# Kernel tuning notes

Measured on AMD Instinct MI355X. Metric: run time of the kernel, lower is better.

Reference implementation:

```python
import jax, jax.numpy as jnp
import numpy as np

D_STATE = 4
DT_RANK = 4  # ceil(64/16)
D_INNER = 64


def conv1d(x, w, b, pad):
    # x: [B,C,L], w: [O,I,K]
    y = jax.lax.conv_general_dilated(x, w, (1,), [(pad, pad)],
                                     dimension_numbers=('NCH', 'OIH', 'NCH'))
    return y + b[None, :, None]


def maxpool2(x):
    B, C, L = x.shape
    return x.reshape(B, C, L // 2, 2).max(-1)


def layernorm(x, g, b):
    m = x.mean(-1, keepdims=True)
    v = ((x - m) ** 2).mean(-1, keepdims=True)
    return (x - m) / jnp.sqrt(v + 1e-5) * g + b


def mamba_block(x, in_w, cv_w, cv_b, xp_w, dt_w, dt_b, A_log, Dp, out_w):
    # x: [B,L,d_model]; d_inner == d_model (expand=1)
    B, L, _ = x.shape
    xz = jnp.einsum('bld,ed->ble', x, in_w)          # [B,L,2*d_inner]
    xi, z = jnp.split(xz, 2, axis=-1)
    # causal depthwise conv, kernel size 2
    xc = jax.lax.conv_general_dilated(xi.transpose(0, 2, 1), cv_w, (1,), [(1, 0)],
                                      feature_group_count=D_INNER,
                                      dimension_numbers=('NCH', 'OIH', 'NCH'))
    u = jax.nn.silu(xc + cv_b[None, :, None]).transpose(0, 2, 1)  # [B,L,d_inner]
    x_dbl = jnp.einsum('bld,ed->ble', u, xp_w)        # [B,L,dt_rank+2*d_state]
    dt, Bm, Cm = jnp.split(x_dbl, [DT_RANK, DT_RANK + D_STATE], axis=-1)
    dt = jax.nn.softplus(jnp.einsum('blr,dr->bld', dt, dt_w) + dt_b)  # [B,L,d_inner]
    A = -jnp.exp(A_log)                               # [d_inner, d_state]
    dA = jnp.exp(dt[..., None] * A)                   # [B,L,d_inner,d_state]
    dBu = dt[..., None] * Bm[:, :, None, :] * u[..., None]

    def step(h, inp):
        dA_t, dBu_t, C_t = inp
        h = dA_t * h + dBu_t                          # [B,d_inner,d_state]
        y = jnp.einsum('bdn,bn->bd', h, C_t)
        return h, y

    h0 = jnp.zeros((B, D_INNER, D_STATE), x.dtype)
    _, ys = jax.lax.scan(step, h0, (dA.transpose(1, 0, 2, 3),
                                    dBu.transpose(1, 0, 2, 3),
                                    Cm.transpose(1, 0, 2)))
    y = ys.transpose(1, 0, 2) + Dp * u                # skip connection D*u
    y = y * jax.nn.silu(z)
    return jnp.einsum('bld,ed->ble', y, out_w)


def setup_inputs() -> dict:
    key = jax.random.key(0)
    ks = jax.random.split(key, 32)
    n = lambda k, s, sc=0.05: (jax.random.normal(k, s, jnp.float32) * sc)
    inp = {
        'x': jax.random.normal(ks[0], (512, 1, 4096), jnp.float32),
        'c1w': n(ks[1], (16, 1, 5), 0.3), 'c1b': n(ks[2], (16,)),
        'c2w': n(ks[3], (32, 16, 5), 0.1), 'c2b': n(ks[4], (32,)),
        'c3w': n(ks[5], (64, 32, 5), 0.08), 'c3b': n(ks[6], (64,)),
        'lw': n(ks[7], (4096, 2048), 0.02), 'lb': n(ks[8], (4096,)),
    }
    A_init = jnp.log(jnp.tile(jnp.arange(1, D_STATE + 1, dtype=jnp.float32), (D_INNER, 1)))
    for i, base in ((1, 9), (2, 20)):
        inp[f'ln{i}g'] = jnp.ones((64,), jnp.float32)
        inp[f'ln{i}b'] = jnp.zeros((64,), jnp.float32)
        inp[f'in{i}w'] = n(ks[base + 0], (2 * D_INNER, 64), 0.08)
        inp[f'cv{i}w'] = n(ks[base + 1], (D_INNER, 1, 2), 0.3)
        inp[f'cv{i}b'] = n(ks[base + 2], (D_INNER,))
        inp[f'xp{i}w'] = n(ks[base + 3], (DT_RANK + 2 * D_STATE, D_INNER), 0.08)
        inp[f'dt{i}w'] = n(ks[base + 4], (D_INNER, DT_RANK), 0.3)
        inp[f'dt{i}b'] = n(ks[base + 5], (D_INNER,), 0.5)
        inp[f'al{i}'] = A_init
        inp[f'dp{i}'] = jnp.ones((D_INNER,), jnp.float32)
        inp[f'ow{i}'] = n(ks[base + 6], (64, D_INNER), 0.08)
    return inp


def reference(x, c1w, c1b, c2w, c2b, c3w, c3b, lw, lb,
              ln1g, ln1b, in1w, cv1w, cv1b, xp1w, dt1w, dt1b, al1, dp1, ow1,
              ln2g, ln2b, in2w, cv2w, cv2b, xp2w, dt2w, dt2b, al2, dp2, ow2):
    B = x.shape[0]
    h = maxpool2(jax.nn.relu(conv1d(x, c1w, c1b, 2)))       # [B,16,L/2]
    h = maxpool2(jax.nn.relu(conv1d(h, c2w, c2b, 2)))       # [B,32,L/4]
    h = jax.nn.relu(conv1d(h, c3w, c3b, 2))                 # [B,64,L/4]
    # AdaptiveAvgPool1d(32): L/4 divisible by 32 -> exact window means
    L4 = h.shape[-1]
    h = h.reshape(B, 64, 32, L4 // 32).mean(-1)             # [B,64,32]
    h = h.reshape(B, -1)                                    # [B,2048]
    h = (h @ lw.T + lb).reshape(B, 64, 64)                  # [B,64,64]
    h = mamba_block(layernorm(h, ln1g, ln1b), in1w, cv1w, cv1b, xp1w, dt1w, dt1b, al1, dp1, ow1)
    h = mamba_block(layernorm(h, ln2g, ln2b), in2w, cv2w, cv2b, xp2w, dt2w, dt2b, al2, dp2, ow2)
    return h
```

## Files before the change

### kernel.cpp

```cpp
#include <hip/hip_runtime.h>
#include <hip/hip_bf16.h>
#include <math.h>

#define NB 512

typedef __attribute__((ext_vector_type(8))) short short8;
typedef __attribute__((ext_vector_type(4))) float f32x4;
union U4 { uint4 u; short8 s8; };
union BF { __hip_bfloat16 h; ushort us; };

__device__ __forceinline__ int swz(int u) { return u ^ ((u >> 3) & 7); }
__device__ __forceinline__ int idx8(int l, int u) { return l * 8 + (u ^ (l & 7)); }

__global__ __launch_bounds__(256) void prep_w(const float* __restrict__ w2,
                                              __hip_bfloat16* __restrict__ w2b,
                                              const float* __restrict__ w3,
                                              __hip_bfloat16* __restrict__ w3b,
                                              const float* __restrict__ in1w,
                                              const float* __restrict__ in2w,
                                              __hip_bfloat16* __restrict__ winb,
                                              const float* __restrict__ ow1,
                                              const float* __restrict__ ow2,
                                              __hip_bfloat16* __restrict__ owb) {
    int i = blockIdx.x * 256 + threadIdx.x;
    if (i < 3072) {
        int c2 = i / 96, rest = i - c2 * 96;
        int tp = rest >> 5, r2 = rest & 31;
        int tl = r2 >> 4, c1 = r2 & 15;
        int tap = tp * 2 + tl;
        float v = (tap < 5) ? w2[c2 * 80 + c1 * 5 + tap] : 0.f;
        w2b[i] = __float2bfloat16(v);
    } else if (i < 13312) {
        int j = i - 3072;
        int c3 = j / 160, rest = j - c3 * 160;
        int kk = rest >> 5, c1 = rest & 31;
        w3b[j] = __float2bfloat16(w3[c3 * 160 + c1 * 5 + kk]);
    } else if (i < 29696) {
        int j = i - 13312;
        winb[j] = __float2bfloat16((j < 8192 ? in1w : in2w)[j & 8191]);
    } else {
        int j = i - 29696;
        owb[j] = __float2bfloat16((j < 4096 ? ow1 : ow2)[j & 4095]);
    }
}

__global__ __launch_bounds__(256) void conv_trunk(const float* __restrict__ x,
                                                  const float* __restrict__ c1w,
                                                  const float* __restrict__ c1b,
                                                  const __hip_bfloat16* __restrict__ w2b,
                                                  const float* __restrict__ c2b,
                                                  const __hip_bfloat16* __restrict__ w3b,
                                                  const float* __restrict__ c3b,
                                                  __hip_bfloat16* __restrict__ h3b) {
    __shared__ uint4 H1u[1088];
    __shared__ uint4 H2u[1088];
    float* xs = (float*)H2u;
    int t = threadIdx.x, h = blockIdx.x, b = blockIdx.y;
    int lane = t & 63, w = t >> 6, m = lane & 15, quad = lane >> 4;
    int p0 = h * 512 - 6;
    int gbase = h * 1024 - 14;

    const float* xb = x + b * 4096;
    for (int i = t; i < 1080; i += 256) {
        int gx = gbase + i;
        xs[i] = (gx >= 0 && gx < 4096) ? xb[gx] : 0.f;
    }
    U4 Bf2[3][2];
    {
        const uint4* wsrc = (const uint4*)w2b;
#pragma unroll
        for (int ct = 0; ct < 2; ++ct)
#pragma unroll
            for (int tp = 0; tp < 3; ++tp)
                Bf2[tp][ct].u = wsrc[(ct * 16 + m) * 12 + tp * 4 + quad];
    }
    float bv2[2];
#pragma unroll
    for (int ct = 0; ct < 2; ++ct) bv2[ct] = c2b[ct * 16 + m];
    float wv[80], bv1[16];
#pragma unroll
    for (int i = 0; i < 80; ++i) wv[i] = c1w[i];
#pragma unroll
    for (int i = 0; i < 16; ++i) bv1[i] = c1b[i];
    __syncthreads();

    for (int r = t; r < 536; r += 256) {
        int p = p0 + r;
        union { uint4 q[2]; __hip_bfloat16 hh[16]; } o;
        if (p >= 0 && p < 2048) {
            const float* s = xs + 2 * r;
            float s0 = s[0], s1 = s[1], s2 = s[2], s3 = s[3], s4 = s[4], s5 = s[5];
#pragma unroll
            for (int c = 0; c < 16; ++c) {
                const float* wr = wv + c * 5;
                float v0 = fmaf(wr[0], s0, fmaf(wr[1], s1, fmaf(wr[2], s2, fmaf(wr[3], s3, fmaf(wr[4], s4, bv1[c])))));
                float v1 = fmaf(wr[0], s1, fmaf(wr[1], s2, fmaf(wr[2], s3, fmaf(wr[3], s4, fmaf(wr[4], s5, bv1[c])))));
                o.hh[c] = __float2bfloat16(fmaxf(fmaxf(v0, v1), 0.f));
            }
        } else {
            o.q[0] = (uint4){0, 0, 0, 0};
            o.q[1] = (uint4){0, 0, 0, 0};
        }
        H1u[swz(2 * r)] = o.q[0];
        H1u[swz(2 * r + 1)] = o.q[1];
    }
    __syncthreads();

    __hip_bfloat16* H2h = (__hip_bfloat16*)H2u;
    for (int g = w; g < 33; g += 4) {
        f32x4 acc[2];
#pragma unroll
        for (int ct = 0; ct < 2; ++ct) acc[ct] = (f32x4){bv2[ct], bv2[ct], bv2[ct], bv2[ct]};
#pragma unroll
        for (int tp = 0; tp < 3; ++tp) {
            int u = 2 * (g * 16 + m + 2 * tp) + quad;
            U4 av; av.u = H1u[swz(u)];
            acc[0] = __builtin_amdgcn_mfma_f32_16x16x32_bf16(av.s8, Bf2[tp][0].s8, acc[0], 0, 0, 0);
            acc[1] = __builtin_amdgcn_mfma_f32_16x16x32_bf16(av.s8, Bf2[tp][1].s8, acc[1], 0, 0, 0);
        }
        int pp = g * 8 + quad * 2;
#pragma unroll
        for (int ct = 0; ct < 2; ++ct) {
            float o0 = fmaxf(fmaxf(acc[ct][0], acc[ct][1]), 0.f);
            float o1 = fmaxf(fmaxf(acc[ct][2], acc[ct][3]), 0.f);
            int ch = ct * 16 + m;
            int u0 = pp * 4 + (ch >> 3);
            H2h[swz(u0) * 8 + (ch & 7)] = __float2bfloat16(o0);
            H2h[swz(u0 + 4) * 8 + (ch & 7)] = __float2bfloat16(o1);
        }
    }
    __syncthreads();
    if (h == 0 && t < 8) H2u[swz((t >> 2) * 4 + (t & 3))] = (uint4){0, 0, 0, 0};
    if (h == 3 && t < 8) H2u[swz((258 + (t >> 2)) * 4 + (t & 3))] = (uint4){0, 0, 0, 0};
    __syncthreads();

    U4 Bf3[5][4];
    {
        const uint4* wsrc = (const uint4*)w3b;
#pragma unroll
        for (int ct = 0; ct < 4; ++ct)
#pragma unroll
            for (int kk = 0; kk < 5; ++kk)
                Bf3[kk][ct].u = wsrc[(ct * 16 + m) * 20 + kk * 4 + quad];
    }
    float bv3[4];
#pragma unroll
    for (int ct = 0; ct < 4; ++ct) bv3[ct] = c3b[ct * 16 + m];

#pragma unroll
    for (int ww = 0; ww < 2; ++ww) {
        int wl = w * 2 + ww;
        float sum[4] = {0.f, 0.f, 0.f, 0.f};
#pragma unroll
        for (int half = 0; half < 2; ++half) {
            int gp = wl * 2 + half;
            f32x4 acc[4];
#pragma unroll
            for (int ct = 0; ct < 4; ++ct) acc[ct] = (f32x4){bv3[ct], bv3[ct], bv3[ct], bv3[ct]};
#pragma unroll
            for (int kk = 0; kk < 5; ++kk) {
                int u = 4 * (gp * 16 + m + kk) + quad;
                U4 av; av.u = H2u[swz(u)];
#pragma unroll
                for (int ct = 0; ct < 4; ++ct)
                    acc[ct] = __builtin_amdgcn_mfma_f32_16x16x32_bf16(av.s8, Bf3[kk][ct].s8, acc[ct], 0, 0, 0);
            }
#pragma unroll
            for (int ct = 0; ct < 4; ++ct) {
                sum[ct] += fmaxf(acc[ct][0], 0.f) + fmaxf(acc[ct][1], 0.f)
                         + fmaxf(acc[ct][2], 0.f) + fmaxf(acc[ct][3], 0.f);
            }
        }
#pragma unroll
        for (int ct = 0; ct < 4; ++ct) {
            float s = sum[ct];
            s += __shfl_xor(s, 16, 64);
            s += __shfl_xor(s, 32, 64);
            sum[ct] = s;
        }
        float sv = (quad == 0) ? sum[0] : (quad == 1) ? sum[1] : (quad == 2) ? sum[2] : sum[3];
        int win = h * 8 + wl;
        h3b[b * 2048 + (quad * 16 + m) * 32 + win] = __float2bfloat16(sv * (1.f / 32.f));
    }
}

__global__ __launch_bounds__(256) void lin_gemm_mfma(const __hip_bfloat16* __restrict__ A,
                                                     const float* __restrict__ Bw,
                                                     const float* __restrict__ bias,
                                                     float* __restrict__ C) {
    __shared__ uint4 A_s[512];
    __shared__ uint4 B_s[512];
    int t = threadIdx.x;
    int col0 = blockIdx.x * 64;
    int row0 = blockIdx.y * 64;
    int w = t >> 6, lane = t & 63;
    int m = lane & 15, quad = lane >> 4;
    int lh = w >> 1, eh = w & 1;

    f32x4 acc[2][2];
#pragma unroll
    for (int li = 0; li < 2; ++li)
#pragma unroll
        for (int ei = 0; ei < 2; ++ei) acc[li][ei] = (f32x4){0.f, 0.f, 0.f, 0.f};

    for (int ki = 0; ki < 32; ++ki) {
        int k0 = ki * 64;
#pragma unroll
        for (int p = 0; p < 2; ++p) {
            int id = p * 256 + t;
            int r = id >> 3, u = id & 7;
            A_s[r * 8 + (u ^ (r & 7))] = *(const uint4*)(A + (row0 + r) * 2048 + k0 + u * 8);
            const float4* s4 = (const float4*)(Bw + (size_t)(col0 + r) * 2048 + k0 + u * 8);
            float4 f0 = s4[0], f1 = s4[1];
            union { uint4 q; __hip_bfloat16 hh[8]; } o;
            o.hh[0] = __float2bfloat16(f0.x); o.hh[1] = __float2bfloat16(f0.y);
            o.hh[2] = __float2bfloat16(f0.z); o.hh[3] = __float2bfloat16(f0.w);
            o.hh[4] = __float2bfloat16(f1.x); o.hh[5] = __float2bfloat16(f1.y);
            o.hh[6] = __float2bfloat16(f1.z); o.hh[7] = __float2bfloat16(f1.w);
            B_s[r * 8 + (u ^ (r & 7))] = o.q;
        }
        __syncthreads();
#pragma unroll
        for (int c = 0; c < 2; ++c) {
            int uu = c * 4 + quad;
            U4 av[2], bv[2];
#pragma unroll
            for (int li = 0; li < 2; ++li) {
                int ra = (lh * 2 + li) * 16 + m;
                av[li].u = A_s[ra * 8 + (uu ^ (ra & 7))];
            }
#pragma unroll
            for (int ei = 0; ei < 2; ++ei) {
                int rb = (eh * 2 + ei) * 16 + m;
                bv[ei].u = B_s[rb * 8 + (uu ^ (rb & 7))];
            }
#pragma unroll
            for (int li = 0; li < 2; ++li)
#pragma unroll
                for (int ei = 0; ei < 2; ++ei)
                    acc[li][ei] = __builtin_amdgcn_mfma_f32_16x16x32_bf16(av[li].s8, bv[ei].s8, acc[li][ei], 0, 0, 0);
        }
        __syncthreads();
    }
#pragma unroll
    for (int li = 0; li < 2; ++li)
#pragma unroll
        for (int ei = 0; ei < 2; ++ei) {
            int col = col0 + (eh * 2 + ei) * 16 + m;
            float bvv = bias[col];
#pragma unroll
            for (int reg = 0; reg < 4; ++reg) {
                int row = row0 + (lh * 2 + li) * 16 + quad * 4 + reg;
                C[row * 4096 + col] = acc[li][ei][reg] + bvv;
            }
        }
}

struct MambaP {
    const float *lng, *lnb, *cvw, *cvb, *xpw, *dtw, *dtb, *al, *dp;
};

__global__ __launch_bounds__(256) void mamba2_kernel(const float* __restrict__ lin,
                                                     const __hip_bfloat16* __restrict__ winb,
                                                     const __hip_bfloat16* __restrict__ owb,
                                                     MambaP p1, MambaP p2,
                                                     float* __restrict__ out) {
    __shared__ float X[64][68];
    __shared__ float XI[64][68];
    __shared__ float DTS[64][68];
    __shared__ float W12[64][14];
    __shared__ uint4 XBu[512];
    int b = blockIdx.x, t = threadIdx.x;
    int lane = t & 63, w = t >> 6, m = lane & 15, quad = lane >> 4;
    int l0 = w * 16;

    {
        const float4* lin4 = (const float4*)(lin + b * 4096);
        for (int i = t; i < 1024; i += 256) {
            float4 v = lin4[i];
            *(float4*)(&X[i >> 4][(i & 15) * 4]) = v;
        }
    }
    __syncthreads();

    for (int blk = 0; blk < 2; ++blk) {
        MambaP P = blk ? p2 : p1;

        {
            int l = t >> 2, q = t & 3;
            float4 xv[4];
            const float4* xr = (const float4*)(&X[l][q * 16]);
#pragma unroll
            for (int j = 0; j < 4; ++j) xv[j] = xr[j];
            float s = 0.f;
#pragma unroll
            for (int j = 0; j < 4; ++j) s += (xv[j].x + xv[j].y) + (xv[j].z + xv[j].w);
            s += __shfl_xor(s, 1, 4);
            s += __shfl_xor(s, 2, 4);
            float mm = s * (1.f / 64.f);
            float v = 0.f;
#pragma unroll
            for (int j = 0; j < 4; ++j) {
                float dx;
                dx = xv[j].x - mm; v = fmaf(dx, dx, v);
                dx = xv[j].y - mm; v = fmaf(dx, dx, v);
                dx = xv[j].z - mm; v = fmaf(dx, dx, v);
                dx = xv[j].w - mm; v = fmaf(dx, dx, v);
            }
            v += __shfl_xor(v, 1, 4);
            v += __shfl_xor(v, 2, 4);
            float rstd = rsqrtf(v * (1.f / 64.f) + 1e-5f);
            const float4* g4 = (const float4*)(P.lng + q * 16);
            const float4* bb4 = (const float4*)(P.lnb + q * 16);
            union { uint4 qq[2]; __hip_bfloat16 hh[16]; } o;
#pragma unroll
            for (int j = 0; j < 4; ++j) {
                float4 g = g4[j], bb = bb4[j];
                o.hh[j * 4 + 0] = __float2bfloat16((xv[j].x - mm) * rstd * g.x + bb.x);
                o.hh[j * 4 + 1] = __float2bfloat16((xv[j].y - mm) * rstd * g.y + bb.y);
                o.hh[j * 4 + 2] = __float2bfloat16((xv[j].z - mm) * rstd * g.z + bb.z);
                o.hh[j * 4 + 3] = __float2bfloat16((xv[j].w - mm) * rstd * g.w + bb.w);
            }
            XBu[idx8(l, q * 2)] = o.qq[0];
            XBu[idx8(l, q * 2 + 1)] = o.qq[1];
        }
        __syncthreads();

        {
            const uint4* wp = (const uint4*)winb + blk * 1024;
            U4 Bf[8][2];
#pragma unroll
            for (int nt = 0; nt < 8; ++nt)
#pragma unroll
                for (int c = 0; c < 2; ++c)
                    Bf[nt][c].u = wp[(nt * 16 + m) * 8 + c * 4 + quad];
            f32x4 acc[8];
#pragma unroll
            for (int nt = 0; nt < 8; ++nt) acc[nt] = (f32x4){0.f, 0.f, 0.f, 0.f};
#pragma unroll
            for (int c = 0; c < 2; ++c) {
                U4 av; av.u = XBu[idx8(l0 + m, c * 4 + quad)];
#pragma unroll
                for (int nt = 0; nt < 8; ++nt)
                    acc[nt] = __builtin_amdgcn_mfma_f32_16x16x32_bf16(av.s8, Bf[nt][c].s8, acc[nt], 0, 0, 0);
            }
#pragma unroll
            for (int nt = 0; nt < 4; ++nt)
#pragma unroll
                for (int reg = 0; reg < 4; ++reg)
                    XI[l0 + quad * 4 + reg][nt * 16 + m] = acc[nt][reg];
#pragma unroll
            for (int nt = 4; nt < 8; ++nt)
#pragma unroll
                for (int reg = 0; reg < 4; ++reg)
                    X[l0 + quad * 4 + reg][(nt - 4) * 16 + m] = acc[nt][reg];
        }
        __syncthreads();

        {
            int d = t & 63, lg = t >> 6;
            int lc = lg * 16;
            float cur[16];
            float prev = (lc == 0) ? 0.f : XI[lc - 1][d];
#pragma unroll
            for (int j = 0; j < 16; ++j) cur[j] = XI[lc + j][d];
            __syncthreads();
            float w0 = P.cvw[d * 2], w1 = P.cvw[d * 2 + 1], cb = P.cvb[d];
#pragma unroll
            for (int j = 0; j < 16; ++j) {
                float xp = (j == 0) ? prev : cur[j - 1];
                float v = fmaf(w0, xp, fmaf(w1, cur[j], cb));
                XI[lc + j][d] = v / (1.f + __expf(-v));
            }
        }
        __syncthreads();

        {
            int l = t & 63, jg = t >> 6;
            float4 xrow[16];
            const float4* xr = (const float4*)(&XI[l][0]);
#pragma unroll
            for (int k4 = 0; k4 < 16; ++k4) xrow[k4] = xr[k4];
#pragma unroll
            for (int jj = 0; jj < 3; ++jj) {
                int j = jg * 3 + jj;
                const float4* wr = (const float4*)(P.xpw + j * 64);
                float a0 = 0.f, a1 = 0.f, a2 = 0.f, a3 = 0.f;
#pragma unroll
                for (int k4 = 0; k4 < 16; ++k4) {
                    float4 wvv = wr[k4];
                    a0 = fmaf(xrow[k4].x, wvv.x, a0);
                    a1 = fmaf(xrow[k4].y, wvv.y, a1);
                    a2 = fmaf(xrow[k4].z, wvv.z, a2);
                    a3 = fmaf(xrow[k4].w, wvv.w, a3);
                }
                float accv = (a0 + a1) + (a2 + a3);
                int slot = (j < 4) ? j : ((j < 8) ? (4 + (j - 4) * 2) : (5 + (j - 8) * 2));
                W12[l][slot] = accv;
            }
        }
        __syncthreads();

        {
            int l = t & 63, dg = t >> 6;
            float d0 = W12[l][0], d1 = W12[l][1], d2 = W12[l][2], d3 = W12[l][3];
#pragma unroll 4
            for (int jj = 0; jj < 16; ++jj) {
                int d = dg * 16 + jj;
                const float4 wvv = *(const float4*)(P.dtw + d * 4);
                float xdt = fmaf(wvv.x, d0, fmaf(wvv.y, d1, fmaf(wvv.z, d2, fmaf(wvv.w, d3, P.dtb[d]))));
                DTS[d][l] = fmaxf(xdt, 0.f) + __logf(1.f + __expf(-fabsf(xdt)));
            }
        }
        __syncthreads();

        {
            int d = t >> 2, n = t & 3;
            float Aval = -__expf(P.al[d * 4 + n]);
            float dpv = P.dp[d];
            const float* dtrow = &DTS[d][0];
            ushort* YBh = (ushort*)XBu;
            float h = 0.f;
#pragma unroll 4
            for (int l = 0; l < 64; ++l) {
                float dtv = dtrow[l];
                float dA = __expf(dtv * Aval);
                float uv = XI[l][d];
                float2 bc = *(const float2*)(&W12[l][4 + n * 2]);
                h = fmaf(dA, h, dtv * bc.x * uv);
                float part = h * bc.y;
                part += __shfl_xor(part, 1, 4);
                part += __shfl_xor(part, 2, 4);
                if (n == 0) {
                    float zv = X[l][d];
                    float yv = part + dpv * uv;
                    float gy = yv * (zv / (1.f + __expf(-zv)));
                    BF cv; cv.h = __float2bfloat16(gy);
                    YBh[idx8(l, d >> 3) * 8 + (d & 7)] = cv.us;
                }
            }
        }
        __syncthreads();

        {
            const uint4* wp = (const uint4*)owb + blk * 512;
            U4 Bf[4][2];
#pragma unroll
            for (int nt = 0; nt < 4; ++nt)
#pragma unroll
                for (int c = 0; c < 2; ++c)
                    Bf[nt][c].u = wp[(nt * 16 + m) * 8 + c * 4 + quad];
            f32x4 acc[4];
#pragma unroll
            for (int nt = 0; nt < 4; ++nt) acc[nt] = (f32x4){0.f, 0.f, 0.f, 0.f};
#pragma unroll
            for (int c = 0; c < 2; ++c) {
                U4 av; av.u = XBu[idx8(l0 + m, c * 4 + quad)];
#pragma unroll
                for (int nt = 0; nt < 4; ++nt)
                    acc[nt] = __builtin_amdgcn_mfma_f32_16x16x32_bf16(av.s8, Bf[nt][c].s8, acc[nt], 0, 0, 0);
            }
            if (blk == 0) {
#pragma unroll
                for (int nt = 0; nt < 4; ++nt)
#pragma unroll
                    for (int reg = 0; reg < 4; ++reg)
                        X[l0 + quad * 4 + reg][nt * 16 + m] = acc[nt][reg];
            } else {
                float* ob = out + b * 4096;
#pragma unroll
                for (int nt = 0; nt < 4; ++nt)
#pragma unroll
                    for (int reg = 0; reg < 4; ++reg)
                        ob[(l0 + quad * 4 + reg) * 64 + nt * 16 + m] = acc[nt][reg];
            }
        }
        __syncthreads();
    }
}

extern "C" void kernel_launch(void* const* d_in, const int* in_sizes, int n_in,
                              void* d_out, int out_size, void* d_ws, size_t ws_size,
                              hipStream_t stream) {
    const float* x   = (const float*)d_in[0];
    const float* c1w = (const float*)d_in[1];
    const float* c1b = (const float*)d_in[2];
    const float* c2w = (const float*)d_in[3];
    const float* c2b = (const float*)d_in[4];
    const float* c3w = (const float*)d_in[5];
    const float* c3b = (const float*)d_in[6];
    const float* lw  = (const float*)d_in[7];
    const float* lb  = (const float*)d_in[8];

    MambaP p1, p2;
    p1.lng = (const float*)d_in[9];  p1.lnb = (const float*)d_in[10];
    p1.cvw = (const float*)d_in[12]; p1.cvb = (const float*)d_in[13];
    p1.xpw = (const float*)d_in[14]; p1.dtw = (const float*)d_in[15];
    p1.dtb = (const float*)d_in[16]; p1.al  = (const float*)d_in[17];
    p1.dp  = (const float*)d_in[18];
    p2.lng = (const float*)d_in[20]; p2.lnb = (const float*)d_in[21];
    p2.cvw = (const float*)d_in[23]; p2.cvb = (const float*)d_in[24];
    p2.xpw = (const float*)d_in[25]; p2.dtw = (const float*)d_in[26];
    p2.dtb = (const float*)d_in[27]; p2.al  = (const float*)d_in[28];
    p2.dp  = (const float*)d_in[29];
    const float* in1w = (const float*)d_in[11];
    const float* in2w = (const float*)d_in[22];
    const float* ow1  = (const float*)d_in[19];
    const float* ow2  = (const float*)d_in[30];

    const size_t MB = 1024 * 1024;
    char* base = (char*)d_ws;
    __hip_bfloat16* h3b  = (__hip_bfloat16*)base;
    float* lin           = (float*)(base + 4 * MB);
    __hip_bfloat16* w2b  = (__hip_bfloat16*)(base + 16 * MB);
    __hip_bfloat16* w3b  = (__hip_bfloat16*)(base + 16 * MB + 64 * 1024);
    __hip_bfloat16* winb = (__hip_bfloat16*)(base + 16 * MB + 256 * 1024);
    __hip_bfloat16* owb  = (__hip_bfloat16*)(base + 16 * MB + 512 * 1024);
    float* outp = (float*)d_out;

    prep_w<<<dim3(148), dim3(256), 0, stream>>>(c2w, w2b, c3w, w3b,
                                                in1w, in2w, winb, ow1, ow2, owb);
    conv_trunk<<<dim3(4, NB), dim3(256), 0, stream>>>(x, c1w, c1b, w2b, c2b, w3b, c3b, h3b);
    lin_gemm_mfma<<<dim3(64, 8), dim3(256), 0, stream>>>(h3b, lw, lb, lin);
    mamba2_kernel<<<dim3(NB), dim3(256), 0, stream>>>(lin, winb, owb, p1, p2, outp);
}
```

Baseline: 267.0 us.

## Prefetch next K tile into registers and widen lin_gemm K-tile to 256

The linear-layer GEMM now processes K in 256-wide tiles instead of 64-wide, using larger shared buffers with a 32-way XOR swizzle. Global loads for the next tile are issued into registers before the MFMA loop on the current tile, so memory latency overlaps compute. This cuts the number of barrier iterations from 32 to 8 per block. The cost is much higher register use for the prefetch buffers (24 vector registers' worth per thread) and 64KB of LDS, which may reduce occupancy.

```diff
diff --git a/kernel.cpp b/kernel.cpp
--- a/kernel.cpp
+++ b/kernel.cpp
@@ -188,8 +188,8 @@
                                                      const float* __restrict__ Bw,
                                                      const float* __restrict__ bias,
                                                      float* __restrict__ C) {
-    __shared__ uint4 A_s[512];
-    __shared__ uint4 B_s[512];
+    __shared__ uint4 A_s[64 * 32];
+    __shared__ uint4 B_s[64 * 32];
     int t = threadIdx.x;
     int col0 = blockIdx.x * 64;
     int row0 = blockIdx.y * 64;
@@ -203,36 +203,56 @@
 #pragma unroll
         for (int ei = 0; ei < 2; ++ei) acc[li][ei] = (f32x4){0.f, 0.f, 0.f, 0.f};
 
-    for (int ki = 0; ki < 32; ++ki) {
-        int k0 = ki * 64;
-#pragma unroll
-        for (int p = 0; p < 2; ++p) {
-            int id = p * 256 + t;
-            int r = id >> 3, u = id & 7;
-            A_s[r * 8 + (u ^ (r & 7))] = *(const uint4*)(A + (row0 + r) * 2048 + k0 + u * 8);
-            const float4* s4 = (const float4*)(Bw + (size_t)(col0 + r) * 2048 + k0 + u * 8);
-            float4 f0 = s4[0], f1 = s4[1];
+    uint4 pa[8];
+    float4 pb[16];
+
+#pragma unroll
+    for (int p = 0; p < 8; ++p) {
+        int id = p * 256 + t, r = id >> 5, u = id & 31;
+        pa[p] = *(const uint4*)(A + (row0 + r) * 2048 + u * 8);
+        const float4* s4 = (const float4*)(Bw + (size_t)(col0 + r) * 2048 + u * 8);
+        pb[2 * p] = s4[0];
+        pb[2 * p + 1] = s4[1];
+    }
+
+    for (int kt = 0; kt < 8; ++kt) {
+#pragma unroll
+        for (int p = 0; p < 8; ++p) {
+            int id = p * 256 + t, r = id >> 5, u = id & 31;
+            A_s[r * 32 + (u ^ (r & 31))] = pa[p];
+            float4 f0 = pb[2 * p], f1 = pb[2 * p + 1];
             union { uint4 q; __hip_bfloat16 hh[8]; } o;
             o.hh[0] = __float2bfloat16(f0.x); o.hh[1] = __float2bfloat16(f0.y);
             o.hh[2] = __float2bfloat16(f0.z); o.hh[3] = __float2bfloat16(f0.w);
             o.hh[4] = __float2bfloat16(f1.x); o.hh[5] = __float2bfloat16(f1.y);
             o.hh[6] = __float2bfloat16(f1.z); o.hh[7] = __float2bfloat16(f1.w);
-            B_s[r * 8 + (u ^ (r & 7))] = o.q;
-        }
-        __syncthreads();
-#pragma unroll
-        for (int c = 0; c < 2; ++c) {
-            int uu = c * 4 + quad;
+            B_s[r * 32 + (u ^ (r & 31))] = o.q;
+        }
+        __syncthreads();
+        if (kt < 7) {
+            int k0 = (kt + 1) * 256;
+#pragma unroll
+            for (int p = 0; p < 8; ++p) {
+                int id = p * 256 + t, r = id >> 5, u = id & 31;
+                pa[p] = *(const uint4*)(A + (row0 + r) * 2048 + k0 + u * 8);
+                const float4* s4 = (const float4*)(Bw + (size_t)(col0 + r) * 2048 + k0 + u * 8);
+                pb[2 * p] = s4[0];
+                pb[2 * p + 1] = s4[1];
+            }
+        }
+#pragma unroll
+        for (int uu = 0; uu < 8; ++uu) {
+            int ua = uu * 4 + quad;
             U4 av[2], bv[2];
 #pragma unroll
             for (int li = 0; li < 2; ++li) {
                 int ra = (lh * 2 + li) * 16 + m;
-                av[li].u = A_s[ra * 8 + (uu ^ (ra & 7))];
+                av[li].u = A_s[ra * 32 + (ua ^ (ra & 31))];
             }
 #pragma unroll
             for (int ei = 0; ei < 2; ++ei) {
                 int rb = (eh * 2 + ei) * 16 + m;
-                bv[ei].u = B_s[rb * 8 + (uu ^ (rb & 7))];
+                bv[ei].u = B_s[rb * 32 + (ua ^ (rb & 31))];
             }
 #pragma unroll
             for (int li = 0; li < 2; ++li)
```

Result: slower. 287.6 us (+7.7%).

## Split-K the linear GEMM four ways and reduce partials in mamba kernel

Applied to the files above, without the earlier changes.

The 512x2048x4096 linear GEMM now splits K into four slices across a third grid dimension, so 2048 blocks run instead of 512. Each slice writes fp32 partial sums to its own workspace buffer. The mamba kernel sums the four partials plus the bias when it loads its input. This raises occupancy across the CUs, at the cost of four times the intermediate write and read traffic and a larger workspace.

```diff
diff --git a/kernel.cpp b/kernel.cpp
--- a/kernel.cpp
+++ b/kernel.cpp
@@ -186,13 +186,13 @@
 
 __global__ __launch_bounds__(256) void lin_gemm_mfma(const __hip_bfloat16* __restrict__ A,
                                                      const float* __restrict__ Bw,
-                                                     const float* __restrict__ bias,
-                                                     float* __restrict__ C) {
+                                                     float* __restrict__ Cp) {
     __shared__ uint4 A_s[512];
     __shared__ uint4 B_s[512];
     int t = threadIdx.x;
     int col0 = blockIdx.x * 64;
     int row0 = blockIdx.y * 64;
+    int ks = blockIdx.z;
     int w = t >> 6, lane = t & 63;
     int m = lane & 15, quad = lane >> 4;
     int lh = w >> 1, eh = w & 1;
@@ -203,8 +203,8 @@
 #pragma unroll
         for (int ei = 0; ei < 2; ++ei) acc[li][ei] = (f32x4){0.f, 0.f, 0.f, 0.f};
 
-    for (int ki = 0; ki < 32; ++ki) {
-        int k0 = ki * 64;
+    for (int ki = 0; ki < 8; ++ki) {
+        int k0 = ks * 512 + ki * 64;
 #pragma unroll
         for (int p = 0; p < 2; ++p) {
             int id = p * 256 + t;
@@ -242,16 +242,16 @@
         }
         __syncthreads();
     }
+    float* Cb = Cp + (size_t)ks * 2097152;
 #pragma unroll
     for (int li = 0; li < 2; ++li)
 #pragma unroll
         for (int ei = 0; ei < 2; ++ei) {
             int col = col0 + (eh * 2 + ei) * 16 + m;
-            float bvv = bias[col];
 #pragma unroll
             for (int reg = 0; reg < 4; ++reg) {
                 int row = row0 + (lh * 2 + li) * 16 + quad * 4 + reg;
-                C[row * 4096 + col] = acc[li][ei][reg] + bvv;
+                Cb[row * 4096 + col] = acc[li][ei][reg];
             }
         }
 }
@@ -260,7 +260,8 @@
     const float *lng, *lnb, *cvw, *cvb, *xpw, *dtw, *dtb, *al, *dp;
 };
 
-__global__ __launch_bounds__(256) void mamba2_kernel(const float* __restrict__ lin,
+__global__ __launch_bounds__(256) void mamba2_kernel(const float* __restrict__ part,
+                                                     const float* __restrict__ lb,
                                                      const __hip_bfloat16* __restrict__ winb,
                                                      const __hip_bfloat16* __restrict__ owb,
                                                      MambaP p1, MambaP p2,
@@ -275,9 +276,18 @@
     int l0 = w * 16;
 
     {
-        const float4* lin4 = (const float4*)(lin + b * 4096);
+        const float4* s0 = (const float4*)(part + (size_t)b * 4096);
+        const float4* s1 = (const float4*)(part + 2097152 + (size_t)b * 4096);
+        const float4* s2 = (const float4*)(part + 2 * 2097152 + (size_t)b * 4096);
+        const float4* s3 = (const float4*)(part + 3 * 2097152 + (size_t)b * 4096);
+        const float4* bb = (const float4*)lb;
         for (int i = t; i < 1024; i += 256) {
-            float4 v = lin4[i];
+            float4 a = s0[i], c = s1[i], d = s2[i], e = s3[i], f = bb[i];
+            float4 v;
+            v.x = ((a.x + c.x) + (d.x + e.x)) + f.x;
+            v.y = ((a.y + c.y) + (d.y + e.y)) + f.y;
+            v.z = ((a.z + c.z) + (d.z + e.z)) + f.z;
+            v.w = ((a.w + c.w) + (d.w + e.w)) + f.w;
             *(float4*)(&X[i >> 4][(i & 15) * 4]) = v;
         }
     }
@@ -428,12 +438,12 @@
                 float uv = XI[l][d];
                 float2 bc = *(const float2*)(&W12[l][4 + n * 2]);
                 h = fmaf(dA, h, dtv * bc.x * uv);
-                float part = h * bc.y;
-                part += __shfl_xor(part, 1, 4);
-                part += __shfl_xor(part, 2, 4);
+                float part2 = h * bc.y;
+                part2 += __shfl_xor(part2, 1, 4);
+                part2 += __shfl_xor(part2, 2, 4);
                 if (n == 0) {
                     float zv = X[l][d];
-                    float yv = part + dpv * uv;
+                    float yv = part2 + dpv * uv;
                     float gy = yv * (zv / (1.f + __expf(-zv)));
                     BF cv; cv.h = __float2bfloat16(gy);
                     YBh[idx8(l, d >> 3) * 8 + (d & 7)] = cv.us;
@@ -511,16 +521,16 @@
     const size_t MB = 1024 * 1024;
     char* base = (char*)d_ws;
     __hip_bfloat16* h3b  = (__hip_bfloat16*)base;
-    float* lin           = (float*)(base + 4 * MB);
-    __hip_bfloat16* w2b  = (__hip_bfloat16*)(base + 16 * MB);
-    __hip_bfloat16* w3b  = (__hip_bfloat16*)(base + 16 * MB + 64 * 1024);
-    __hip_bfloat16* winb = (__hip_bfloat16*)(base + 16 * MB + 256 * 1024);
-    __hip_bfloat16* owb  = (__hip_bfloat16*)(base + 16 * MB + 512 * 1024);
+    float* part          = (float*)(base + 4 * MB);
+    __hip_bfloat16* w2b  = (__hip_bfloat16*)(base + 40 * MB);
+    __hip_bfloat16* w3b  = (__hip_bfloat16*)(base + 40 * MB + 64 * 1024);
+    __hip_bfloat16* winb = (__hip_bfloat16*)(base + 40 * MB + 256 * 1024);
+    __hip_bfloat16* owb  = (__hip_bfloat16*)(base + 40 * MB + 512 * 1024);
     float* outp = (float*)d_out;
 
     prep_w<<<dim3(148), dim3(256), 0, stream>>>(c2w, w2b, c3w, w3b,
                                                 in1w, in2w, winb, ow1, ow2, owb);
     conv_trunk<<<dim3(4, NB), dim3(256), 0, stream>>>(x, c1w, c1b, w2b, c2b, w3b, c3b, h3b);
-    lin_gemm_mfma<<<dim3(64, 8), dim3(256), 0, stream>>>(h3b, lw, lb, lin);
-    mamba2_kernel<<<dim3(NB), dim3(256), 0, stream>>>(lin, winb, owb, p1, p2, outp);
+    lin_gemm_mfma<<<dim3(64, 8, 4), dim3(256), 0, stream>>>(h3b, lw, part);
+    mamba2_kernel<<<dim3(NB), dim3(256), 0, stream>>>(part, lb, winb, owb, p1, p2, outp);
 }
```

Result: faster. 242.9 us (-9.0%).
